# Kernel optimization log

Measured on AMD Instinct MI355X. Metric: run time of the kernel, lower is better.

Reference implementation:

```python
import jax, jax.numpy as jnp
import numpy as np

VOCAB = 100000
EMB = 100
HID = 100
CTX_LEN = 60          # must equal MAX_DESC_LEN for linear_1 to fit
FACT_LEN = 20
DESC_LEN = 60


def setup_inputs() -> dict:
    key = jax.random.key(0)
    ks = jax.random.split(key, 12)
    s = 0.05
    context = jax.random.randint(ks[0], (CTX_LEN, FACT_LEN), 1, VOCAB)
    fact_lengths = jax.random.randint(ks[1], (CTX_LEN,), 1, FACT_LEN)
    description = jax.random.randint(ks[2], (DESC_LEN,), 1, VOCAB)
    emb_ctx = jax.random.normal(ks[3], (VOCAB, EMB), jnp.float32) * s
    emb_ctx = emb_ctx.at[0].set(0.0)  # padding_idx=0
    emb_dec = jax.random.normal(ks[4], (VOCAB, EMB), jnp.float32) * s
    emb_dec = emb_dec.at[0].set(0.0)
    w1 = jax.random.normal(ks[5], (HID, CTX_LEN * HID), jnp.float32) * s
    b1 = jax.random.normal(ks[6], (HID,), jnp.float32) * s
    w_ih = jax.random.normal(ks[7], (3 * HID, EMB), jnp.float32) * s
    w_hh = jax.random.normal(ks[8], (3 * HID, HID), jnp.float32) * s
    b_ih = jax.random.normal(ks[9], (3 * HID,), jnp.float32) * s
    b_hh = jax.random.normal(ks[10], (3 * HID,), jnp.float32) * s
    w_out = jax.random.normal(ks[11], (VOCAB, HID), jnp.float32) * s
    b_out = jnp.zeros((VOCAB,), jnp.float32)
    return {"context": context, "fact_lengths": fact_lengths, "description": description,
            "emb_ctx": emb_ctx, "emb_dec": emb_dec, "w1": w1, "b1": b1,
            "w_ih": w_ih, "w_hh": w_hh, "b_ih": b_ih, "b_hh": b_hh,
            "w_out": w_out, "b_out": b_out}


def _forward(context, description, emb_ctx, emb_dec, w1, b1,
             w_ih, w_hh, b_ih, b_hh, w_out, b_out):
    # ---- InputModule: embed + positional fact encoder ----
    emb = emb_ctx[context]                       # [CTX_LEN, FACT_LEN, EMB]
    slen, elen = FACT_LEN, EMB
    s = jnp.arange(slen, dtype=jnp.float32) / (slen - 1)   # [slen]
    e = jnp.arange(elen, dtype=jnp.float32) / (elen - 1)   # [elen]
    l = 1.0 - s[:, None] - e[None, :] * (1.0 - 2.0 * s[:, None])  # [slen, elen]
    facts = jnp.sum(emb * l[None], axis=1)       # [CTX_LEN, EMB]

    # ---- initial decoder hidden from flattened facts ----
    h0 = facts.reshape(1, -1) @ w1.T + b1        # [1, HID]

    x0 = emb_dec[1][None, :]                     # SOS token embedding [1, EMB]

    def step(carry, tok):
        h, x = carry
        gi = x @ w_ih.T + b_ih                   # [1, 3H]
        gh = h @ w_hh.T + b_hh
        i_r, i_z, i_n = jnp.split(gi, 3, axis=-1)
        h_r, h_z, h_n = jnp.split(gh, 3, axis=-1)
        r = jax.nn.sigmoid(i_r + h_r)
        z = jax.nn.sigmoid(i_z + h_z)
        n = jnp.tanh(i_n + r * h_n)
        h_new = (1.0 - z) * n + z * h            # [1, HID]
        logits = h_new @ w_out.T + b_out         # [1, VOCAB]
        logp = jax.nn.log_softmax(logits, axis=-1)
        loss_t = -logp[0, tok]                   # NLLLoss, batch 1
        x_next = emb_dec[tok][None, :]           # teacher forcing
        return (h_new, x_next), loss_t

    (_, _), losses = jax.lax.scan(step, (h0, x0), description)
    return jnp.sum(losses).reshape(1)            # matches torch FloatTensor([.])


def reference(context, fact_lengths, description, emb_ctx, emb_dec, w1, b1,
              w_ih, w_hh, b_ih, b_hh, w_out, b_out):
    # fact_lengths is unused by the original forward (PositionalFactEncoder ignores it)
    return _forward(context, description, emb_ctx, emb_dec, w1, b1,
                    w_ih, w_hh, b_ih, b_hh, w_out, b_out)
```

## Files before the change

kernel.cpp:

```cpp
#include <hip/hip_runtime.h>
#include <hip/hip_bf16.h>
#include <math.h>

#define VOCAB 100000
#define EMB 100
#define HID 100
#define CTX_LEN 60
#define FACT_LEN 20
#define DESC_LEN 60
#define NCHUNK (VOCAB / 16)
#define NWAVES 1024

#define WS_FACTS 0
#define WS_X     6000
#define WS_H0    12000
#define WS_GI    12160
#define WS_H     30160
#define WS_MS    36864

typedef __attribute__((ext_vector_type(8))) short short8;
typedef __attribute__((ext_vector_type(4))) float f32x4;

static __device__ __forceinline__ unsigned short f2bf(float f) {
    union { float f; unsigned u; } x; x.f = f;
    unsigned r = (x.u + 0x7FFFu + ((x.u >> 16) & 1u)) >> 16;
    return (unsigned short)r;
}

__global__ __launch_bounds__(128) void k1_prep(const int* __restrict__ context,
                                               const int* __restrict__ desc,
                                               const float* __restrict__ emb_ctx,
                                               const float* __restrict__ emb_dec,
                                               float* __restrict__ ws,
                                               float* __restrict__ out) {
    int b = blockIdx.x, tid = threadIdx.x;
    if (b < 60) {
        __shared__ int toks[20];
        if (tid < 20) toks[tid] = context[b * 20 + tid];
        __syncthreads();
        if (tid < 100) {
            float ef = tid * (1.f / 99.f);
            float acc = 0.f;
            #pragma unroll
            for (int s = 0; s < 20; s++) {
                float sf = s * (1.f / 19.f);
                float l = 1.f - sf - ef * (1.f - 2.f * sf);
                acc = fmaf(emb_ctx[toks[s] * 100 + tid], l, acc);
            }
            ws[WS_FACTS + b * 100 + tid] = acc;
        }
    } else {
        int t = b - 60;
        int tok = (t == 0) ? 1 : desc[t - 1];
        if (tid < 100) ws[WS_X + t * 100 + tid] = emb_dec[tok * 100 + tid];
        if (b == 60 && tid == 0) out[0] = 0.f;
    }
}

__global__ __launch_bounds__(320) void k2_h0_gi(const float* __restrict__ w1,
                                                const float* __restrict__ b1,
                                                const float* __restrict__ w_ih,
                                                const float* __restrict__ b_ih,
                                                float* __restrict__ ws) {
    int b = blockIdx.x, tid = threadIdx.x;
    if (b < 100) {
        __shared__ float red[320];
        const float* facts = ws + WS_FACTS;
        const float* wr = w1 + b * 6000;
        float p = 0.f;
        for (int k = tid; k < 6000; k += 320) p = fmaf(facts[k], wr[k], p);
        red[tid] = p; __syncthreads();
        if (tid < 64) red[tid] += red[256 + tid];
        __syncthreads();
        for (int st = 128; st > 0; st >>= 1) {
            if (tid < st) red[tid] += red[tid + st];
            __syncthreads();
        }
        if (tid == 0) ws[WS_H0 + b] = red[0] + b1[b];
    } else {
        int t = b - 100;
        __shared__ float xs[100];
        if (tid < 100) xs[tid] = ws[WS_X + t * 100 + tid];
        __syncthreads();
        if (tid < 300) {
            float p = b_ih[tid];
            const float* wr = w_ih + tid * 100;
            #pragma unroll 4
            for (int k = 0; k < 100; k++) p = fmaf(wr[k], xs[k], p);
            ws[WS_GI + t * 300 + tid] = p;
        }
    }
}

__global__ __launch_bounds__(256, 1) void k3_gru(const float* __restrict__ w_hh,
                                                 const float* __restrict__ b_hh,
                                                 float* __restrict__ ws) {
    __shared__ __align__(16) float gi_lds[18000];
    __shared__ __align__(16) float H_lds[6000];
    __shared__ __align__(16) unsigned short h_bf[2][128];

    const int tid = threadIdx.x;
    const int wave = tid >> 6, lane = tid & 63;
    const int q = lane >> 4, n = lane & 15;
    const int L = lane & 31;
    const int j = wave * 32 + L;
    const bool gate_lane = (lane < 32) && (j < 100);

    short8 bfr[3][2][4];
    #pragma unroll
    for (int s = 0; s < 3; s++) {
        #pragma unroll
        for (int c = 0; c < 2; c++) {
            const int jrow = wave * 32 + c * 16 + n;
            const float* wr = w_hh + (s * 100 + jrow) * 100;
            #pragma unroll
            for (int kt = 0; kt < 4; kt++) {
                int k0 = kt * 32 + q * 8;
                float va[8];
                #pragma unroll
                for (int jj = 0; jj < 8; jj++) va[jj] = 0.f;
                if (jrow < 100) {
                    if (k0 + 4 <= 100) {
                        float4 a = *(const float4*)(wr + k0);
                        va[0] = a.x; va[1] = a.y; va[2] = a.z; va[3] = a.w;
                    }
                    if (k0 + 8 <= 100) {
                        float4 b = *(const float4*)(wr + k0 + 4);
                        va[4] = b.x; va[5] = b.y; va[6] = b.z; va[7] = b.w;
                    }
                }
                short8 f;
                #pragma unroll
                for (int jj = 0; jj < 8; jj++) f[jj] = (short)f2bf(va[jj]);
                bfr[s][c][kt] = f;
            }
        }
    }

    {
        const float4* src = (const float4*)(ws + WS_GI);
        float4* dst = (float4*)gi_lds;
        for (int k = tid; k < 4500; k += 256) dst[k] = src[k];
    }

    float hreg = 0.f, bh0 = 0.f, bh1 = 0.f, bh2 = 0.f;
    if (gate_lane) {
        hreg = ws[WS_H0 + j];
        bh0 = b_hh[j]; bh1 = b_hh[100 + j]; bh2 = b_hh[200 + j];
    }
    if (tid < 128) {
        h_bf[0][tid] = (tid < 100) ? f2bf(ws[WS_H0 + tid]) : (unsigned short)0;
        h_bf[1][tid] = 0;
    }
    __syncthreads();

    const int js = (j < 100) ? j : 0;
    for (int t = 0; t < 60; t++) {
        const int rb = t & 1;
        float gir = gi_lds[t * 300 + js];
        float giz = gi_lds[t * 300 + 100 + js];
        float gin = gi_lds[t * 300 + 200 + js];

        short8 afr[4];
        #pragma unroll
        for (int kt = 0; kt < 4; kt++)
            afr[kt] = *(const short8*)&h_bf[rb][kt * 32 + q * 8];

        f32x4 acc[3][2];
        #pragma unroll
        for (int s = 0; s < 3; s++) {
            #pragma unroll
            for (int c = 0; c < 2; c++) {
                f32x4 a = {0.f, 0.f, 0.f, 0.f};
                a = __builtin_amdgcn_mfma_f32_16x16x32_bf16(afr[0], bfr[s][c][0], a, 0, 0, 0);
                a = __builtin_amdgcn_mfma_f32_16x16x32_bf16(afr[1], bfr[s][c][1], a, 0, 0, 0);
                a = __builtin_amdgcn_mfma_f32_16x16x32_bf16(afr[2], bfr[s][c][2], a, 0, 0, 0);
                a = __builtin_amdgcn_mfma_f32_16x16x32_bf16(afr[3], bfr[s][c][3], a, 0, 0, 0);
                acc[s][c] = a;
            }
        }

        if (gate_lane) {
            const int cc = L >> 4;
            float ghr = (cc ? acc[0][1][0] : acc[0][0][0]) + bh0;
            float ghz = (cc ? acc[1][1][0] : acc[1][0][0]) + bh1;
            float ghn = (cc ? acc[2][1][0] : acc[2][0][0]) + bh2;
            float r = 1.f / (1.f + __expf(-(gir + ghr)));
            float z = 1.f / (1.f + __expf(-(giz + ghz)));
            float a2 = fmaf(r, ghn, gin);
            float tt = __expf(-2.f * fabsf(a2));
            float nn = copysignf((1.f - tt) / (1.f + tt), a2);
            hreg = (1.f - z) * nn + z * hreg;
            h_bf[rb ^ 1][j] = f2bf(hreg);
            H_lds[t * 100 + j] = hreg;
        }
        __syncthreads();
    }

    {
        const float4* src = (const float4*)H_lds;
        float4* dst = (float4*)(ws + WS_H);
        for (int k = tid; k < 1500; k += 256) dst[k] = src[k];
    }
}

__global__ __launch_bounds__(256, 1) void k4_logits(const float* __restrict__ w_out,
                                                    const float* __restrict__ b_out,
                                                    float* __restrict__ ws) {
    const float* H = ws + WS_H;
    float* ms = ws + WS_MS;
    const int lane = threadIdx.x & 63;
    const int gw = blockIdx.x * 4 + (threadIdx.x >> 6);
    const int q = lane >> 4, n = lane & 15;
    const int k_base = q * 8;

    short8 afr[4][4];
    #pragma unroll
    for (int mt = 0; mt < 4; mt++) {
        int m = mt * 16 + n;
        #pragma unroll
        for (int kt = 0; kt < 4; kt++) {
            int k0 = kt * 32 + k_base;
            float va[8];
            #pragma unroll
            for (int jj = 0; jj < 8; jj++) va[jj] = 0.f;
            if (m < 60) {
                if (k0 + 4 <= 100) {
                    float4 a = *(const float4*)(H + m * 100 + k0);
                    va[0] = a.x; va[1] = a.y; va[2] = a.z; va[3] = a.w;
                }
                if (k0 + 8 <= 100) {
                    float4 b = *(const float4*)(H + m * 100 + k0 + 4);
                    va[4] = b.x; va[5] = b.y; va[6] = b.z; va[7] = b.w;
                }
            }
            short8 f;
            #pragma unroll
            for (int jj = 0; jj < 8; jj++) f[jj] = (short)f2bf(va[jj]);
            afr[mt][kt] = f;
        }
    }

    float mS[16], sS[16];
    #pragma unroll
    for (int i = 0; i < 16; i++) { mS[i] = -3.0e38f; sS[i] = 0.f; }

    for (int c = gw; c < NCHUNK; c += NWAVES) {
        int row = c * 16 + n;
        short8 bfr[4];
        #pragma unroll
        for (int kt = 0; kt < 4; kt++) {
            int k0 = kt * 32 + k_base;
            float va[8];
            #pragma unroll
            for (int jj = 0; jj < 8; jj++) va[jj] = 0.f;
            if (k0 + 4 <= 100) {
                float4 a = *(const float4*)(w_out + row * 100 + k0);
                va[0] = a.x; va[1] = a.y; va[2] = a.z; va[3] = a.w;
            }
            if (k0 + 8 <= 100) {
                float4 b = *(const float4*)(w_out + row * 100 + k0 + 4);
                va[4] = b.x; va[5] = b.y; va[6] = b.z; va[7] = b.w;
            }
            short8 f;
            #pragma unroll
            for (int jj = 0; jj < 8; jj++) f[jj] = (short)f2bf(va[jj]);
            bfr[kt] = f;
        }
        float bo = b_out[row];
        #pragma unroll
        for (int mt = 0; mt < 4; mt++) {
            f32x4 acc = {0.f, 0.f, 0.f, 0.f};
            acc = __builtin_amdgcn_mfma_f32_16x16x32_bf16(afr[mt][0], bfr[0], acc, 0, 0, 0);
            acc = __builtin_amdgcn_mfma_f32_16x16x32_bf16(afr[mt][1], bfr[1], acc, 0, 0, 0);
            acc = __builtin_amdgcn_mfma_f32_16x16x32_bf16(afr[mt][2], bfr[2], acc, 0, 0, 0);
            acc = __builtin_amdgcn_mfma_f32_16x16x32_bf16(afr[mt][3], bfr[3], acc, 0, 0, 0);
            #pragma unroll
            for (int reg = 0; reg < 4; reg++) {
                float x = acc[reg] + bo;
                int i = mt * 4 + reg;
                float mo = mS[i];
                float mn = fmaxf(mo, x);
                sS[i] = sS[i] * __expf(mo - mn) + __expf(x - mn);
                mS[i] = mn;
            }
        }
    }

    #pragma unroll
    for (int i = 0; i < 16; i++) {
        float m = mS[i], s = sS[i];
        #pragma unroll
        for (int off = 1; off < 16; off <<= 1) {
            float m2 = __shfl_xor(m, off);
            float s2 = __shfl_xor(s, off);
            float mn = fmaxf(m, m2);
            s = s * __expf(m - mn) + s2 * __expf(m2 - mn);
            m = mn;
        }
        mS[i] = m; sS[i] = s;
    }
    if (n == 0) {
        #pragma unroll
        for (int mt = 0; mt < 4; mt++) {
            #pragma unroll
            for (int reg = 0; reg < 4; reg++) {
                int t = mt * 16 + q * 4 + reg;
                int i = mt * 4 + reg;
                if (t < 60) {
                    float2 val; val.x = mS[i]; val.y = sS[i];
                    ((float2*)ms)[t * NWAVES + gw] = val;
                }
            }
        }
    }
}

__global__ __launch_bounds__(256) void k5_final(const int* __restrict__ desc,
                                                const float* __restrict__ w_out,
                                                const float* __restrict__ b_out,
                                                const float* __restrict__ ws,
                                                float* __restrict__ out) {
    int t = blockIdx.x, tid = threadIdx.x;
    __shared__ float sm[256], ss[256], sd[256];
    const float2* ms = (const float2*)(ws + WS_MS);
    float m = -3.0e38f, s = 0.f;
    for (int i = tid; i < NWAVES; i += 256) {
        float2 p = ms[t * NWAVES + i];
        float mn = fmaxf(m, p.x);
        s = s * __expf(m - mn) + p.y * __expf(p.x - mn);
        m = mn;
    }
    sm[tid] = m; ss[tid] = s; __syncthreads();
    for (int st = 128; st > 0; st >>= 1) {
        if (tid < st) {
            float mo = sm[tid], so = ss[tid];
            float m2 = sm[tid + st], s2 = ss[tid + st];
            float mn = fmaxf(mo, m2);
            sm[tid] = mn;
            ss[tid] = so * __expf(mo - mn) + s2 * __expf(m2 - mn);
        }
        __syncthreads();
    }
    int tok = desc[t];
    float p = 0.f;
    if (tid < 100) p = ws[WS_H + t * 100 + tid] * w_out[tok * 100 + tid];
    sd[tid] = p; __syncthreads();
    for (int st = 128; st > 0; st >>= 1) {
        if (tid < st) sd[tid] += sd[tid + st];
        __syncthreads();
    }
    if (tid == 0) {
        float logit = sd[0] + b_out[tok];
        float loss = sm[0] + logf(ss[0]) - logit;
        atomicAdd(out, loss);
    }
}

extern "C" void kernel_launch(void* const* d_in, const int* in_sizes, int n_in,
                              void* d_out, int out_size, void* d_ws, size_t ws_size,
                              hipStream_t stream) {
    const int*   context = (const int*)d_in[0];
    const int*   desc    = (const int*)d_in[2];
    const float* emb_ctx = (const float*)d_in[3];
    const float* emb_dec = (const float*)d_in[4];
    const float* w1      = (const float*)d_in[5];
    const float* b1      = (const float*)d_in[6];
    const float* w_ih    = (const float*)d_in[7];
    const float* w_hh    = (const float*)d_in[8];
    const float* b_ih    = (const float*)d_in[9];
    const float* b_hh    = (const float*)d_in[10];
    const float* w_out   = (const float*)d_in[11];
    const float* b_out   = (const float*)d_in[12];
    float* out = (float*)d_out;
    float* ws  = (float*)d_ws;

    k1_prep  <<<120, 128, 0, stream>>>(context, desc, emb_ctx, emb_dec, ws, out);
    k2_h0_gi <<<160, 320, 0, stream>>>(w1, b1, w_ih, b_ih, ws);
    k3_gru   <<<1,   256, 0, stream>>>(w_hh, b_hh, ws);
    k4_logits<<<256, 256, 0, stream>>>(w_out, b_out, ws);
    k5_final <<<60,  256, 0, stream>>>(desc, w_out, b_out, ws, out);
}
```

Before: 200.3 us.

## Fuse all stages into one persistent kernel and overlap GRU with w_out conversion

Replaces the five kernel launches with a single persistent kernel of 224 blocks that separates stages with a software grid barrier built on atomics. While block 0 runs the serial GRU recurrence, the other blocks convert w_out to bf16 in MFMA fragment order in workspace, so the logits stage reads pre-packed bf16 weights instead of converting fp32 on the fly. This aims to remove launch gaps and hide the w_out conversion behind the serial GRU, at the cost of an extra write and read of a bf16 copy of w_out, a hipMemset for the barrier counter, and reliance on all blocks being co-resident.

```diff
diff --git a/kernel.cpp b/kernel.cpp
--- a/kernel.cpp
+++ b/kernel.cpp
@@ -9,14 +9,19 @@
 #define FACT_LEN 20
 #define DESC_LEN 60
 #define NCHUNK (VOCAB / 16)
-#define NWAVES 1024
-
-#define WS_FACTS 0
-#define WS_X     6000
-#define WS_H0    12000
-#define WS_GI    12160
-#define WS_H     30160
+#define GRID 224
+#define BLOCK 320
+#define WPB 5
+#define NWAVES (GRID * WPB)
+
+#define WS_BAR   0
+#define WS_FACTS 64
+#define WS_X     6144
+#define WS_H0    12288
+#define WS_GI    12416
+#define WS_H     30464
 #define WS_MS    36864
+#define WS_WBF   262144
 
 typedef __attribute__((ext_vector_type(8))) short short8;
 typedef __attribute__((ext_vector_type(4))) float f32x4;
@@ -27,15 +32,42 @@
     return (unsigned short)r;
 }
 
-__global__ __launch_bounds__(128) void k1_prep(const int* __restrict__ context,
-                                               const int* __restrict__ desc,
-                                               const float* __restrict__ emb_ctx,
-                                               const float* __restrict__ emb_dec,
-                                               float* __restrict__ ws,
-                                               float* __restrict__ out) {
-    int b = blockIdx.x, tid = threadIdx.x;
+static __device__ __forceinline__ void grid_sync(float* ws) {
+    __syncthreads();
+    if (threadIdx.x == 0) {
+        unsigned* cnt = (unsigned*)ws;
+        unsigned* gen = (unsigned*)ws + 16;
+        __threadfence();
+        unsigned g = __hip_atomic_load(gen, __ATOMIC_RELAXED, __HIP_MEMORY_SCOPE_AGENT);
+        unsigned a = __hip_atomic_fetch_add(cnt, 1u, __ATOMIC_ACQ_REL, __HIP_MEMORY_SCOPE_AGENT);
+        if (a == GRID - 1) {
+            __hip_atomic_store(cnt, 0u, __ATOMIC_RELAXED, __HIP_MEMORY_SCOPE_AGENT);
+            __hip_atomic_store(gen, g + 1u, __ATOMIC_RELEASE, __HIP_MEMORY_SCOPE_AGENT);
+        } else {
+            while (__hip_atomic_load(gen, __ATOMIC_ACQUIRE, __HIP_MEMORY_SCOPE_AGENT) == g)
+                __builtin_amdgcn_s_sleep(2);
+        }
+        __threadfence();
+    }
+    __syncthreads();
+}
+
+__global__ __launch_bounds__(BLOCK, 1) void mega(
+    const int* __restrict__ context, const int* __restrict__ desc,
+    const float* __restrict__ emb_ctx, const float* __restrict__ emb_dec,
+    const float* __restrict__ w1, const float* __restrict__ b1,
+    const float* __restrict__ w_ih, const float* __restrict__ b_ih,
+    const float* __restrict__ w_hh, const float* __restrict__ b_hh,
+    const float* __restrict__ w_out, const float* __restrict__ b_out,
+    float* __restrict__ ws, float* __restrict__ out)
+{
+    __shared__ __align__(16) float smem[24128];
+    const int b = blockIdx.x, tid = threadIdx.x;
+    const int lane = tid & 63, wave = tid >> 6;
+    const int q = lane >> 4, n = lane & 15;
+
     if (b < 60) {
-        __shared__ int toks[20];
+        int* toks = (int*)smem;
         if (tid < 20) toks[tid] = context[b * 20 + tid];
         __syncthreads();
         if (tid < 100) {
@@ -49,22 +81,17 @@
             }
             ws[WS_FACTS + b * 100 + tid] = acc;
         }
-    } else {
+    } else if (b < 120) {
         int t = b - 60;
         int tok = (t == 0) ? 1 : desc[t - 1];
         if (tid < 100) ws[WS_X + t * 100 + tid] = emb_dec[tok * 100 + tid];
-        if (b == 60 && tid == 0) out[0] = 0.f;
-    }
-}
-
-__global__ __launch_bounds__(320) void k2_h0_gi(const float* __restrict__ w1,
-                                                const float* __restrict__ b1,
-                                                const float* __restrict__ w_ih,
-                                                const float* __restrict__ b_ih,
-                                                float* __restrict__ ws) {
-    int b = blockIdx.x, tid = threadIdx.x;
+    } else if (b == 120 && tid == 0) {
+        out[0] = 0.f;
+    }
+    grid_sync(ws);
+
     if (b < 100) {
-        __shared__ float red[320];
+        float* red = smem;
         const float* facts = ws + WS_FACTS;
         const float* wr = w1 + b * 6000;
         float p = 0.f;
@@ -77,9 +104,9 @@
             __syncthreads();
         }
         if (tid == 0) ws[WS_H0 + b] = red[0] + b1[b];
-    } else {
+    } else if (b < 160) {
         int t = b - 100;
-        __shared__ float xs[100];
+        float* xs = smem;
         if (tid < 100) xs[tid] = ws[WS_X + t * 100 + tid];
         __syncthreads();
         if (tid < 300) {
@@ -90,270 +117,276 @@
             ws[WS_GI + t * 300 + tid] = p;
         }
     }
-}
-
-__global__ __launch_bounds__(256, 1) void k3_gru(const float* __restrict__ w_hh,
-                                                 const float* __restrict__ b_hh,
-                                                 float* __restrict__ ws) {
-    __shared__ __align__(16) float gi_lds[18000];
-    __shared__ __align__(16) float H_lds[6000];
-    __shared__ __align__(16) unsigned short h_bf[2][128];
-
-    const int tid = threadIdx.x;
-    const int wave = tid >> 6, lane = tid & 63;
-    const int q = lane >> 4, n = lane & 15;
-    const int L = lane & 31;
-    const int j = wave * 32 + L;
-    const bool gate_lane = (lane < 32) && (j < 100);
-
-    short8 bfr[3][2][4];
-    #pragma unroll
-    for (int s = 0; s < 3; s++) {
+    grid_sync(ws);
+
+    if (b == 0) {
+        float* gi_lds = smem;
+        float* H_lds  = smem + 18000;
+        unsigned short (*h_bf)[128] = (unsigned short (*)[128])(smem + 24000);
+        const int L = lane & 31;
+        const int j = wave * 32 + L;
+        const bool gruwave = (wave < 4);
+        const bool gate_lane = gruwave && (lane < 32) && (j < 100);
+
+        short8 bfr[3][2][4];
+        if (gruwave) {
+            #pragma unroll
+            for (int s = 0; s < 3; s++) {
+                #pragma unroll
+                for (int c = 0; c < 2; c++) {
+                    const int jrow = wave * 32 + c * 16 + n;
+                    const float* wr = w_hh + (s * 100 + jrow) * 100;
+                    #pragma unroll
+                    for (int kt = 0; kt < 4; kt++) {
+                        int k0 = kt * 32 + q * 8;
+                        float va[8];
+                        #pragma unroll
+                        for (int jj = 0; jj < 8; jj++) va[jj] = 0.f;
+                        if (jrow < 100) {
+                            if (k0 + 4 <= 100) {
+                                float4 a = *(const float4*)(wr + k0);
+                                va[0] = a.x; va[1] = a.y; va[2] = a.z; va[3] = a.w;
+                            }
+                            if (k0 + 8 <= 100) {
+                                float4 a = *(const float4*)(wr + k0 + 4);
+                                va[4] = a.x; va[5] = a.y; va[6] = a.z; va[7] = a.w;
+                            }
+                        }
+                        short8 f;
+                        #pragma unroll
+                        for (int jj = 0; jj < 8; jj++) f[jj] = (short)f2bf(va[jj]);
+                        bfr[s][c][kt] = f;
+                    }
+                }
+            }
+        }
+
+        {
+            const float4* src = (const float4*)(ws + WS_GI);
+            float4* dst = (float4*)gi_lds;
+            for (int k = tid; k < 4500; k += 320) dst[k] = src[k];
+        }
+
+        float hreg = 0.f, bh0 = 0.f, bh1 = 0.f, bh2 = 0.f;
+        if (gate_lane) {
+            hreg = ws[WS_H0 + j];
+            bh0 = b_hh[j]; bh1 = b_hh[100 + j]; bh2 = b_hh[200 + j];
+        }
+        if (tid < 128) {
+            h_bf[0][tid] = (tid < 100) ? f2bf(ws[WS_H0 + tid]) : (unsigned short)0;
+            h_bf[1][tid] = 0;
+        }
+        __syncthreads();
+
+        const int js = (gruwave && j < 100) ? j : 0;
+        for (int t = 0; t < 60; t++) {
+            const int rb = t & 1;
+            if (gruwave) {
+                float gir = gi_lds[t * 300 + js];
+                float giz = gi_lds[t * 300 + 100 + js];
+                float gin = gi_lds[t * 300 + 200 + js];
+
+                short8 afr[4];
+                #pragma unroll
+                for (int kt = 0; kt < 4; kt++)
+                    afr[kt] = *(const short8*)&h_bf[rb][kt * 32 + q * 8];
+
+                f32x4 acc[3][2];
+                #pragma unroll
+                for (int s = 0; s < 3; s++) {
+                    #pragma unroll
+                    for (int c = 0; c < 2; c++) {
+                        f32x4 a = {0.f, 0.f, 0.f, 0.f};
+                        a = __builtin_amdgcn_mfma_f32_16x16x32_bf16(afr[0], bfr[s][c][0], a, 0, 0, 0);
+                        a = __builtin_amdgcn_mfma_f32_16x16x32_bf16(afr[1], bfr[s][c][1], a, 0, 0, 0);
+                        a = __builtin_amdgcn_mfma_f32_16x16x32_bf16(afr[2], bfr[s][c][2], a, 0, 0, 0);
+                        a = __builtin_amdgcn_mfma_f32_16x16x32_bf16(afr[3], bfr[s][c][3], a, 0, 0, 0);
+                        acc[s][c] = a;
+                    }
+                }
+
+                if (gate_lane) {
+                    const int cc = L >> 4;
+                    float ghr = (cc ? acc[0][1][0] : acc[0][0][0]) + bh0;
+                    float ghz = (cc ? acc[1][1][0] : acc[1][0][0]) + bh1;
+                    float ghn = (cc ? acc[2][1][0] : acc[2][0][0]) + bh2;
+                    float r = 1.f / (1.f + __expf(-(gir + ghr)));
+                    float z = 1.f / (1.f + __expf(-(giz + ghz)));
+                    float a2 = fmaf(r, ghn, gin);
+                    float tt = __expf(-2.f * fabsf(a2));
+                    float nn = copysignf((1.f - tt) / (1.f + tt), a2);
+                    hreg = (1.f - z) * nn + z * hreg;
+                    h_bf[rb ^ 1][j] = f2bf(hreg);
+                    H_lds[t * 100 + j] = hreg;
+                }
+            }
+            __syncthreads();
+        }
+
+        {
+            const float4* src = (const float4*)H_lds;
+            float4* dst = (float4*)(ws + WS_H);
+            for (int k = tid; k < 1500; k += 320) dst[k] = src[k];
+        }
+    } else {
+        short8* wbf = (short8*)(ws + WS_WBF);
+        for (int it = (b - 1) * WPB + wave; it < NCHUNK * 4; it += (GRID - 1) * WPB) {
+            int c = it >> 2, kt = it & 3;
+            const float* wr = w_out + (c * 16 + n) * 100;
+            int k0 = kt * 32 + q * 8;
+            float va[8];
+            #pragma unroll
+            for (int jj = 0; jj < 8; jj++) va[jj] = 0.f;
+            if (k0 + 4 <= 100) {
+                float4 a = *(const float4*)(wr + k0);
+                va[0] = a.x; va[1] = a.y; va[2] = a.z; va[3] = a.w;
+            }
+            if (k0 + 8 <= 100) {
+                float4 a = *(const float4*)(wr + k0 + 4);
+                va[4] = a.x; va[5] = a.y; va[6] = a.z; va[7] = a.w;
+            }
+            short8 f;
+            #pragma unroll
+            for (int jj = 0; jj < 8; jj++) f[jj] = (short)f2bf(va[jj]);
+            wbf[(c * 4 + kt) * 64 + lane] = f;
+        }
+    }
+    grid_sync(ws);
+
+    {
+        const float* H = ws + WS_H;
+        float* ms = ws + WS_MS;
+        const short8* wbf = (const short8*)(ws + WS_WBF);
+        const int gw = b * WPB + wave;
+        const int k_base = q * 8;
+
+        short8 afr[4][4];
         #pragma unroll
-        for (int c = 0; c < 2; c++) {
-            const int jrow = wave * 32 + c * 16 + n;
-            const float* wr = w_hh + (s * 100 + jrow) * 100;
+        for (int mt = 0; mt < 4; mt++) {
+            int m = mt * 16 + n;
             #pragma unroll
             for (int kt = 0; kt < 4; kt++) {
-                int k0 = kt * 32 + q * 8;
+                int k0 = kt * 32 + k_base;
                 float va[8];
                 #pragma unroll
                 for (int jj = 0; jj < 8; jj++) va[jj] = 0.f;
-                if (jrow < 100) {
+                if (m < 60) {
                     if (k0 + 4 <= 100) {
-                        float4 a = *(const float4*)(wr + k0);
+                        float4 a = *(const float4*)(H + m * 100 + k0);
                         va[0] = a.x; va[1] = a.y; va[2] = a.z; va[3] = a.w;
                     }
                     if (k0 + 8 <= 100) {
-                        float4 b = *(const float4*)(wr + k0 + 4);
-                        va[4] = b.x; va[5] = b.y; va[6] = b.z; va[7] = b.w;
+                        float4 a = *(const float4*)(H + m * 100 + k0 + 4);
+                        va[4] = a.x; va[5] = a.y; va[6] = a.z; va[7] = a.w;
                     }
                 }
                 short8 f;
                 #pragma unroll
                 for (int jj = 0; jj < 8; jj++) f[jj] = (short)f2bf(va[jj]);
-                bfr[s][c][kt] = f;
-            }
-        }
-    }
-
-    {
-        const float4* src = (const float4*)(ws + WS_GI);
-        float4* dst = (float4*)gi_lds;
-        for (int k = tid; k < 4500; k += 256) dst[k] = src[k];
-    }
-
-    float hreg = 0.f, bh0 = 0.f, bh1 = 0.f, bh2 = 0.f;
-    if (gate_lane) {
-        hreg = ws[WS_H0 + j];
-        bh0 = b_hh[j]; bh1 = b_hh[100 + j]; bh2 = b_hh[200 + j];
-    }
-    if (tid < 128) {
-        h_bf[0][tid] = (tid < 100) ? f2bf(ws[WS_H0 + tid]) : (unsigned short)0;
-        h_bf[1][tid] = 0;
-    }
-    __syncthreads();
-
-    const int js = (j < 100) ? j : 0;
-    for (int t = 0; t < 60; t++) {
-        const int rb = t & 1;
-        float gir = gi_lds[t * 300 + js];
-        float giz = gi_lds[t * 300 + 100 + js];
-        float gin = gi_lds[t * 300 + 200 + js];
-
-        short8 afr[4];
+                afr[mt][kt] = f;
+            }
+        }
+
+        float mS[16], sS[16];
         #pragma unroll
-        for (int kt = 0; kt < 4; kt++)
-            afr[kt] = *(const short8*)&h_bf[rb][kt * 32 + q * 8];
-
-        f32x4 acc[3][2];
+        for (int i = 0; i < 16; i++) { mS[i] = -3.0e38f; sS[i] = 0.f; }
+
+        for (int c = gw; c < NCHUNK; c += NWAVES) {
+            int row = c * 16 + n;
+            short8 bw0 = wbf[(c * 4 + 0) * 64 + lane];
+            short8 bw1 = wbf[(c * 4 + 1) * 64 + lane];
+            short8 bw2 = wbf[(c * 4 + 2) * 64 + lane];
+            short8 bw3 = wbf[(c * 4 + 3) * 64 + lane];
+            float bo = b_out[row];
+            #pragma unroll
+            for (int mt = 0; mt < 4; mt++) {
+                f32x4 acc = {0.f, 0.f, 0.f, 0.f};
+                acc = __builtin_amdgcn_mfma_f32_16x16x32_bf16(afr[mt][0], bw0, acc, 0, 0, 0);
+                acc = __builtin_amdgcn_mfma_f32_16x16x32_bf16(afr[mt][1], bw1, acc, 0, 0, 0);
+                acc = __builtin_amdgcn_mfma_f32_16x16x32_bf16(afr[mt][2], bw2, acc, 0, 0, 0);
+                acc = __builtin_amdgcn_mfma_f32_16x16x32_bf16(afr[mt][3], bw3, acc, 0, 0, 0);
+                #pragma unroll
+                for (int reg = 0; reg < 4; reg++) {
+                    float x = acc[reg] + bo;
+                    int i = mt * 4 + reg;
+                    float mo = mS[i];
+                    float mn = fmaxf(mo, x);
+                    sS[i] = sS[i] * __expf(mo - mn) + __expf(x - mn);
+                    mS[i] = mn;
+                }
+            }
+        }
+
         #pragma unroll
-        for (int s = 0; s < 3; s++) {
-            #pragma unroll
-            for (int c = 0; c < 2; c++) {
-                f32x4 a = {0.f, 0.f, 0.f, 0.f};
-                a = __builtin_amdgcn_mfma_f32_16x16x32_bf16(afr[0], bfr[s][c][0], a, 0, 0, 0);
-                a = __builtin_amdgcn_mfma_f32_16x16x32_bf16(afr[1], bfr[s][c][1], a, 0, 0, 0);
-                a = __builtin_amdgcn_mfma_f32_16x16x32_bf16(afr[2], bfr[s][c][2], a, 0, 0, 0);
-                a = __builtin_amdgcn_mfma_f32_16x16x32_bf16(afr[3], bfr[s][c][3], a, 0, 0, 0);
-                acc[s][c] = a;
-            }
-        }
-
-        if (gate_lane) {
-            const int cc = L >> 4;
-            float ghr = (cc ? acc[0][1][0] : acc[0][0][0]) + bh0;
-            float ghz = (cc ? acc[1][1][0] : acc[1][0][0]) + bh1;
-            float ghn = (cc ? acc[2][1][0] : acc[2][0][0]) + bh2;
-            float r = 1.f / (1.f + __expf(-(gir + ghr)));
-            float z = 1.f / (1.f + __expf(-(giz + ghz)));
-            float a2 = fmaf(r, ghn, gin);
-            float tt = __expf(-2.f * fabsf(a2));
-            float nn = copysignf((1.f - tt) / (1.f + tt), a2);
-            hreg = (1.f - z) * nn + z * hreg;
-            h_bf[rb ^ 1][j] = f2bf(hreg);
-            H_lds[t * 100 + j] = hreg;
-        }
-        __syncthreads();
-    }
-
-    {
-        const float4* src = (const float4*)H_lds;
-        float4* dst = (float4*)(ws + WS_H);
-        for (int k = tid; k < 1500; k += 256) dst[k] = src[k];
-    }
-}
-
-__global__ __launch_bounds__(256, 1) void k4_logits(const float* __restrict__ w_out,
-                                                    const float* __restrict__ b_out,
-                                                    float* __restrict__ ws) {
-    const float* H = ws + WS_H;
-    float* ms = ws + WS_MS;
-    const int lane = threadIdx.x & 63;
-    const int gw = blockIdx.x * 4 + (threadIdx.x >> 6);
-    const int q = lane >> 4, n = lane & 15;
-    const int k_base = q * 8;
-
-    short8 afr[4][4];
-    #pragma unroll
-    for (int mt = 0; mt < 4; mt++) {
-        int m = mt * 16 + n;
-        #pragma unroll
-        for (int kt = 0; kt < 4; kt++) {
-            int k0 = kt * 32 + k_base;
-            float va[8];
-            #pragma unroll
-            for (int jj = 0; jj < 8; jj++) va[jj] = 0.f;
-            if (m < 60) {
-                if (k0 + 4 <= 100) {
-                    float4 a = *(const float4*)(H + m * 100 + k0);
-                    va[0] = a.x; va[1] = a.y; va[2] = a.z; va[3] = a.w;
-                }
-                if (k0 + 8 <= 100) {
-                    float4 b = *(const float4*)(H + m * 100 + k0 + 4);
-                    va[4] = b.x; va[5] = b.y; va[6] = b.z; va[7] = b.w;
-                }
-            }
-            short8 f;
-            #pragma unroll
-            for (int jj = 0; jj < 8; jj++) f[jj] = (short)f2bf(va[jj]);
-            afr[mt][kt] = f;
-        }
-    }
-
-    float mS[16], sS[16];
-    #pragma unroll
-    for (int i = 0; i < 16; i++) { mS[i] = -3.0e38f; sS[i] = 0.f; }
-
-    for (int c = gw; c < NCHUNK; c += NWAVES) {
-        int row = c * 16 + n;
-        short8 bfr[4];
-        #pragma unroll
-        for (int kt = 0; kt < 4; kt++) {
-            int k0 = kt * 32 + k_base;
-            float va[8];
-            #pragma unroll
-            for (int jj = 0; jj < 8; jj++) va[jj] = 0.f;
-            if (k0 + 4 <= 100) {
-                float4 a = *(const float4*)(w_out + row * 100 + k0);
-                va[0] = a.x; va[1] = a.y; va[2] = a.z; va[3] = a.w;
-            }
-            if (k0 + 8 <= 100) {
-                float4 b = *(const float4*)(w_out + row * 100 + k0 + 4);
-                va[4] = b.x; va[5] = b.y; va[6] = b.z; va[7] = b.w;
-            }
-            short8 f;
-            #pragma unroll
-            for (int jj = 0; jj < 8; jj++) f[jj] = (short)f2bf(va[jj]);
-            bfr[kt] = f;
-        }
-        float bo = b_out[row];
-        #pragma unroll
-        for (int mt = 0; mt < 4; mt++) {
-            f32x4 acc = {0.f, 0.f, 0.f, 0.f};
-            acc = __builtin_amdgcn_mfma_f32_16x16x32_bf16(afr[mt][0], bfr[0], acc, 0, 0, 0);
-            acc = __builtin_amdgcn_mfma_f32_16x16x32_bf16(afr[mt][1], bfr[1], acc, 0, 0, 0);
-            acc = __builtin_amdgcn_mfma_f32_16x16x32_bf16(afr[mt][2], bfr[2], acc, 0, 0, 0);
-            acc = __builtin_amdgcn_mfma_f32_16x16x32_bf16(afr[mt][3], bfr[3], acc, 0, 0, 0);
-            #pragma unroll
-            for (int reg = 0; reg < 4; reg++) {
-                float x = acc[reg] + bo;
-                int i = mt * 4 + reg;
-                float mo = mS[i];
-                float mn = fmaxf(mo, x);
-                sS[i] = sS[i] * __expf(mo - mn) + __expf(x - mn);
-                mS[i] = mn;
-            }
-        }
-    }
-
-    #pragma unroll
-    for (int i = 0; i < 16; i++) {
-        float m = mS[i], s = sS[i];
-        #pragma unroll
-        for (int off = 1; off < 16; off <<= 1) {
-            float m2 = __shfl_xor(m, off);
-            float s2 = __shfl_xor(s, off);
-            float mn = fmaxf(m, m2);
-            s = s * __expf(m - mn) + s2 * __expf(m2 - mn);
-            m = mn;
-        }
-        mS[i] = m; sS[i] = s;
-    }
-    if (n == 0) {
-        #pragma unroll
-        for (int mt = 0; mt < 4; mt++) {
-            #pragma unroll
-            for (int reg = 0; reg < 4; reg++) {
-                int t = mt * 16 + q * 4 + reg;
-                int i = mt * 4 + reg;
-                if (t < 60) {
-                    float2 val; val.x = mS[i]; val.y = sS[i];
-                    ((float2*)ms)[t * NWAVES + gw] = val;
-                }
-            }
-        }
-    }
-}
-
-__global__ __launch_bounds__(256) void k5_final(const int* __restrict__ desc,
-                                                const float* __restrict__ w_out,
-                                                const float* __restrict__ b_out,
-                                                const float* __restrict__ ws,
-                                                float* __restrict__ out) {
-    int t = blockIdx.x, tid = threadIdx.x;
-    __shared__ float sm[256], ss[256], sd[256];
-    const float2* ms = (const float2*)(ws + WS_MS);
-    float m = -3.0e38f, s = 0.f;
-    for (int i = tid; i < NWAVES; i += 256) {
-        float2 p = ms[t * NWAVES + i];
-        float mn = fmaxf(m, p.x);
-        s = s * __expf(m - mn) + p.y * __expf(p.x - mn);
-        m = mn;
-    }
-    sm[tid] = m; ss[tid] = s; __syncthreads();
-    for (int st = 128; st > 0; st >>= 1) {
-        if (tid < st) {
-            float mo = sm[tid], so = ss[tid];
-            float m2 = sm[tid + st], s2 = ss[tid + st];
-            float mn = fmaxf(mo, m2);
-            sm[tid] = mn;
-            ss[tid] = so * __expf(mo - mn) + s2 * __expf(m2 - mn);
-        }
-        __syncthreads();
-    }
-    int tok = desc[t];
-    float p = 0.f;
-    if (tid < 100) p = ws[WS_H + t * 100 + tid] * w_out[tok * 100 + tid];
-    sd[tid] = p; __syncthreads();
-    for (int st = 128; st > 0; st >>= 1) {
-        if (tid < st) sd[tid] += sd[tid + st];
-        __syncthreads();
-    }
-    if (tid == 0) {
-        float logit = sd[0] + b_out[tok];
-        float loss = sm[0] + logf(ss[0]) - logit;
-        atomicAdd(out, loss);
+        for (int i = 0; i < 16; i++) {
+            float m = mS[i], s = sS[i];
+            #pragma unroll
+            for (int off = 1; off < 16; off <<= 1) {
+                float m2 = __shfl_xor(m, off);
+                float s2 = __shfl_xor(s, off);
+                float mn = fmaxf(m, m2);
+                s = s * __expf(m - mn) + s2 * __expf(m2 - mn);
+                m = mn;
+            }
+            mS[i] = m; sS[i] = s;
+        }
+        if (n == 0) {
+            #pragma unroll
+            for (int mt = 0; mt < 4; mt++) {
+                #pragma unroll
+                for (int reg = 0; reg < 4; reg++) {
+                    int t = mt * 16 + q * 4 + reg;
+                    int i = mt * 4 + reg;
+                    if (t < 60) {
+                        float2 val; val.x = mS[i]; val.y = sS[i];
+                        ((float2*)ms)[t * NWAVES + gw] = val;
+                    }
+                }
+            }
+        }
+    }
+    grid_sync(ws);
+
+    if (b < 60) {
+        const int t = b;
+        float* sm  = smem;
+        float* ssm = smem + 320;
+        float* sd  = smem + 640;
+        const float2* msp = (const float2*)(ws + WS_MS);
+        float m = -3.0e38f, s = 0.f;
+        if (tid < 256) {
+            for (int i = tid; i < NWAVES; i += 256) {
+                float2 p2 = msp[t * NWAVES + i];
+                float mn = fmaxf(m, p2.x);
+                s = s * __expf(m - mn) + p2.y * __expf(p2.x - mn);
+                m = mn;
+            }
+            sm[tid] = m; ssm[tid] = s;
+        }
+        __syncthreads();
+        for (int st = 128; st > 0; st >>= 1) {
+            if (tid < st) {
+                float mo = sm[tid], so = ssm[tid];
+                float m2 = sm[tid + st], s2 = ssm[tid + st];
+                float mn = fmaxf(mo, m2);
+                sm[tid] = mn;
+                ssm[tid] = so * __expf(mo - mn) + s2 * __expf(m2 - mn);
+            }
+            __syncthreads();
+        }
+        int tok = desc[t];
+        float p = 0.f;
+        if (tid < 100) p = ws[WS_H + t * 100 + tid] * w_out[tok * 100 + tid];
+        if (tid < 256) sd[tid] = p;
+        __syncthreads();
+        for (int st = 128; st > 0; st >>= 1) {
+            if (tid < st) sd[tid] += sd[tid + st];
+            __syncthreads();
+        }
+        if (tid == 0) {
+            float logit = sd[0] + b_out[tok];
+            atomicAdd(out, sm[0] + logf(ssm[0]) - logit);
+        }
     }
 }
 
@@ -375,9 +408,7 @@
     float* out = (float*)d_out;
     float* ws  = (float*)d_ws;
 
-    k1_prep  <<<120, 128, 0, stream>>>(context, desc, emb_ctx, emb_dec, ws, out);
-    k2_h0_gi <<<160, 320, 0, stream>>>(w1, b1, w_ih, b_ih, ws);
-    k3_gru   <<<1,   256, 0, stream>>>(w_hh, b_hh, ws);
-    k4_logits<<<256, 256, 0, stream>>>(w_out, b_out, ws);
-    k5_final <<<60,  256, 0, stream>>>(desc, w_out, b_out, ws, out);
+    hipMemsetAsync(ws, 0, 128, stream);
+    mega<<<GRID, BLOCK, 0, stream>>>(context, desc, emb_ctx, emb_dec, w1, b1,
+                                     w_ih, b_ih, w_hh, b_hh, w_out, b_out, ws, out);
 }
```

Result: slower. 338.5 us (+69.0%).

## Overlap w_out bf16 conversion with serial GRU and merge prep kernels

Applied to the files above, without the earlier changes.

Merges the embedding/fact prep kernel into the h0/gi kernel, so every h0 block recomputes facts redundantly but one launch is saved. Extra blocks of the GRU kernel convert w_out into a pre-swizzled bf16 MFMA layout in the workspace while block 0 runs the serial recurrence, so the logits kernel loads ready fragments instead of converting fp32. The logits grid changes to 224 blocks, and the atomic loss sum becomes a per-step buffer plus a tiny final kernel. This adds a 20MB bf16 write and re-read, and the facts computation is repeated per h0 block.

```diff
diff --git a/kernel.cpp b/kernel.cpp
--- a/kernel.cpp
+++ b/kernel.cpp
@@ -9,14 +9,15 @@
 #define FACT_LEN 20
 #define DESC_LEN 60
 #define NCHUNK (VOCAB / 16)
-#define NWAVES 1024
-
-#define WS_FACTS 0
-#define WS_X     6000
-#define WS_H0    12000
-#define WS_GI    12160
-#define WS_H     30160
-#define WS_MS    36864
+#define GRID_BC 224
+#define NWAVES_C (GRID_BC * 4)
+
+#define WS_H0    0
+#define WS_GI    128
+#define WS_H     18176
+#define WS_LOSS  24176
+#define WS_MS    24256
+#define WS_WBF   262144
 
 typedef __attribute__((ext_vector_type(8))) short short8;
 typedef __attribute__((ext_vector_type(4))) float f32x4;
@@ -27,45 +28,35 @@
     return (unsigned short)r;
 }
 
-__global__ __launch_bounds__(128) void k1_prep(const int* __restrict__ context,
-                                               const int* __restrict__ desc,
-                                               const float* __restrict__ emb_ctx,
-                                               const float* __restrict__ emb_dec,
-                                               float* __restrict__ ws,
-                                               float* __restrict__ out) {
-    int b = blockIdx.x, tid = threadIdx.x;
-    if (b < 60) {
-        __shared__ int toks[20];
-        if (tid < 20) toks[tid] = context[b * 20 + tid];
-        __syncthreads();
-        if (tid < 100) {
-            float ef = tid * (1.f / 99.f);
+__global__ __launch_bounds__(320) void kA(const int* __restrict__ context,
+                                          const int* __restrict__ desc,
+                                          const float* __restrict__ emb_ctx,
+                                          const float* __restrict__ emb_dec,
+                                          const float* __restrict__ w1,
+                                          const float* __restrict__ b1,
+                                          const float* __restrict__ w_ih,
+                                          const float* __restrict__ b_ih,
+                                          float* __restrict__ ws) {
+    const int b = blockIdx.x, tid = threadIdx.x;
+    if (b < 100) {
+        __shared__ int toks[1200];
+        __shared__ float facts[6000];
+        __shared__ float red[320];
+        for (int i = tid; i < 1200; i += 320) toks[i] = context[i];
+        __syncthreads();
+        for (int idx = tid; idx < 6000; idx += 320) {
+            int fb = idx / 100, e = idx - fb * 100;
+            float ef = e * (1.f / 99.f);
             float acc = 0.f;
             #pragma unroll
             for (int s = 0; s < 20; s++) {
                 float sf = s * (1.f / 19.f);
                 float l = 1.f - sf - ef * (1.f - 2.f * sf);
-                acc = fmaf(emb_ctx[toks[s] * 100 + tid], l, acc);
-            }
-            ws[WS_FACTS + b * 100 + tid] = acc;
-        }
-    } else {
-        int t = b - 60;
-        int tok = (t == 0) ? 1 : desc[t - 1];
-        if (tid < 100) ws[WS_X + t * 100 + tid] = emb_dec[tok * 100 + tid];
-        if (b == 60 && tid == 0) out[0] = 0.f;
-    }
-}
-
-__global__ __launch_bounds__(320) void k2_h0_gi(const float* __restrict__ w1,
-                                                const float* __restrict__ b1,
-                                                const float* __restrict__ w_ih,
-                                                const float* __restrict__ b_ih,
-                                                float* __restrict__ ws) {
-    int b = blockIdx.x, tid = threadIdx.x;
-    if (b < 100) {
-        __shared__ float red[320];
-        const float* facts = ws + WS_FACTS;
+                acc = fmaf(emb_ctx[toks[fb * 20 + s] * 100 + e], l, acc);
+            }
+            facts[idx] = acc;
+        }
+        __syncthreads();
         const float* wr = w1 + b * 6000;
         float p = 0.f;
         for (int k = tid; k < 6000; k += 320) p = fmaf(facts[k], wr[k], p);
@@ -78,9 +69,10 @@
         }
         if (tid == 0) ws[WS_H0 + b] = red[0] + b1[b];
     } else {
-        int t = b - 100;
+        const int t = b - 100;
+        const int tok = (t == 0) ? 1 : desc[t - 1];
         __shared__ float xs[100];
-        if (tid < 100) xs[tid] = ws[WS_X + t * 100 + tid];
+        if (tid < 100) xs[tid] = emb_dec[tok * 100 + tid];
         __syncthreads();
         if (tid < 300) {
             float p = b_ih[tid];
@@ -92,16 +84,43 @@
     }
 }
 
-__global__ __launch_bounds__(256, 1) void k3_gru(const float* __restrict__ w_hh,
-                                                 const float* __restrict__ b_hh,
-                                                 float* __restrict__ ws) {
-    __shared__ __align__(16) float gi_lds[18000];
-    __shared__ __align__(16) float H_lds[6000];
-    __shared__ __align__(16) unsigned short h_bf[2][128];
-
-    const int tid = threadIdx.x;
-    const int wave = tid >> 6, lane = tid & 63;
+__global__ __launch_bounds__(256, 1) void kB(const float* __restrict__ w_hh,
+                                             const float* __restrict__ b_hh,
+                                             const float* __restrict__ w_out,
+                                             float* __restrict__ ws) {
+    __shared__ __align__(16) float smem[24128];
+    const int b = blockIdx.x, tid = threadIdx.x;
+    const int lane = tid & 63, wave = tid >> 6;
     const int q = lane >> 4, n = lane & 15;
+
+    if (b != 0) {
+        short8* wbf = (short8*)(ws + WS_WBF);
+        for (int it = (b - 1) * 4 + wave; it < NCHUNK * 4; it += 223 * 4) {
+            int c = it >> 2, kt = it & 3;
+            const float* wr = w_out + (c * 16 + n) * 100;
+            int k0 = kt * 32 + q * 8;
+            float va[8];
+            #pragma unroll
+            for (int jj = 0; jj < 8; jj++) va[jj] = 0.f;
+            if (k0 + 4 <= 100) {
+                float4 a = *(const float4*)(wr + k0);
+                va[0] = a.x; va[1] = a.y; va[2] = a.z; va[3] = a.w;
+            }
+            if (k0 + 8 <= 100) {
+                float4 a = *(const float4*)(wr + k0 + 4);
+                va[4] = a.x; va[5] = a.y; va[6] = a.z; va[7] = a.w;
+            }
+            short8 f;
+            #pragma unroll
+            for (int jj = 0; jj < 8; jj++) f[jj] = (short)f2bf(va[jj]);
+            wbf[(c * 4 + kt) * 64 + lane] = f;
+        }
+        return;
+    }
+
+    float* gi_lds = smem;
+    float* H_lds  = smem + 18000;
+    unsigned short (*h_bf)[128] = (unsigned short (*)[128])(smem + 24000);
     const int L = lane & 31;
     const int j = wave * 32 + L;
     const bool gate_lane = (lane < 32) && (j < 100);
@@ -125,8 +144,8 @@
                         va[0] = a.x; va[1] = a.y; va[2] = a.z; va[3] = a.w;
                     }
                     if (k0 + 8 <= 100) {
-                        float4 b = *(const float4*)(wr + k0 + 4);
-                        va[4] = b.x; va[5] = b.y; va[6] = b.z; va[7] = b.w;
+                        float4 a = *(const float4*)(wr + k0 + 4);
+                        va[4] = a.x; va[5] = a.y; va[6] = a.z; va[7] = a.w;
                     }
                 }
                 short8 f;
@@ -204,14 +223,15 @@
     }
 }
 
-__global__ __launch_bounds__(256, 1) void k4_logits(const float* __restrict__ w_out,
-                                                    const float* __restrict__ b_out,
-                                                    float* __restrict__ ws) {
+__global__ __launch_bounds__(256, 1) void kC(const float* __restrict__ b_out,
+                                             float* __restrict__ ws) {
     const float* H = ws + WS_H;
     float* ms = ws + WS_MS;
-    const int lane = threadIdx.x & 63;
-    const int gw = blockIdx.x * 4 + (threadIdx.x >> 6);
+    const short8* wbf = (const short8*)(ws + WS_WBF);
+    const int tid = threadIdx.x;
+    const int lane = tid & 63, wave = tid >> 6;
     const int q = lane >> 4, n = lane & 15;
+    const int gw = blockIdx.x * 4 + wave;
     const int k_base = q * 8;
 
     short8 afr[4][4];
@@ -230,8 +250,8 @@
                     va[0] = a.x; va[1] = a.y; va[2] = a.z; va[3] = a.w;
                 }
                 if (k0 + 8 <= 100) {
-                    float4 b = *(const float4*)(H + m * 100 + k0 + 4);
-                    va[4] = b.x; va[5] = b.y; va[6] = b.z; va[7] = b.w;
+                    float4 a = *(const float4*)(H + m * 100 + k0 + 4);
+                    va[4] = a.x; va[5] = a.y; va[6] = a.z; va[7] = a.w;
                 }
             }
             short8 f;
@@ -245,36 +265,20 @@
     #pragma unroll
     for (int i = 0; i < 16; i++) { mS[i] = -3.0e38f; sS[i] = 0.f; }
 
-    for (int c = gw; c < NCHUNK; c += NWAVES) {
+    for (int c = gw; c < NCHUNK; c += NWAVES_C) {
         int row = c * 16 + n;
-        short8 bfr[4];
-        #pragma unroll
-        for (int kt = 0; kt < 4; kt++) {
-            int k0 = kt * 32 + k_base;
-            float va[8];
-            #pragma unroll
-            for (int jj = 0; jj < 8; jj++) va[jj] = 0.f;
-            if (k0 + 4 <= 100) {
-                float4 a = *(const float4*)(w_out + row * 100 + k0);
-                va[0] = a.x; va[1] = a.y; va[2] = a.z; va[3] = a.w;
-            }
-            if (k0 + 8 <= 100) {
-                float4 b = *(const float4*)(w_out + row * 100 + k0 + 4);
-                va[4] = b.x; va[5] = b.y; va[6] = b.z; va[7] = b.w;
-            }
-            short8 f;
-            #pragma unroll
-            for (int jj = 0; jj < 8; jj++) f[jj] = (short)f2bf(va[jj]);
-            bfr[kt] = f;
-        }
+        short8 bw0 = wbf[(c * 4 + 0) * 64 + lane];
+        short8 bw1 = wbf[(c * 4 + 1) * 64 + lane];
+        short8 bw2 = wbf[(c * 4 + 2) * 64 + lane];
+        short8 bw3 = wbf[(c * 4 + 3) * 64 + lane];
         float bo = b_out[row];
         #pragma unroll
         for (int mt = 0; mt < 4; mt++) {
             f32x4 acc = {0.f, 0.f, 0.f, 0.f};
-            acc = __builtin_amdgcn_mfma_f32_16x16x32_bf16(afr[mt][0], bfr[0], acc, 0, 0, 0);
-            acc = __builtin_amdgcn_mfma_f32_16x16x32_bf16(afr[mt][1], bfr[1], acc, 0, 0, 0);
-            acc = __builtin_amdgcn_mfma_f32_16x16x32_bf16(afr[mt][2], bfr[2], acc, 0, 0, 0);
-            acc = __builtin_amdgcn_mfma_f32_16x16x32_bf16(afr[mt][3], bfr[3], acc, 0, 0, 0);
+            acc = __builtin_amdgcn_mfma_f32_16x16x32_bf16(afr[mt][0], bw0, acc, 0, 0, 0);
+            acc = __builtin_amdgcn_mfma_f32_16x16x32_bf16(afr[mt][1], bw1, acc, 0, 0, 0);
+            acc = __builtin_amdgcn_mfma_f32_16x16x32_bf16(afr[mt][2], bw2, acc, 0, 0, 0);
+            acc = __builtin_amdgcn_mfma_f32_16x16x32_bf16(afr[mt][3], bw3, acc, 0, 0, 0);
             #pragma unroll
             for (int reg = 0; reg < 4; reg++) {
                 float x = acc[reg] + bo;
@@ -309,26 +313,25 @@
                 int i = mt * 4 + reg;
                 if (t < 60) {
                     float2 val; val.x = mS[i]; val.y = sS[i];
-                    ((float2*)ms)[t * NWAVES + gw] = val;
+                    ((float2*)ms)[t * NWAVES_C + gw] = val;
                 }
             }
         }
     }
 }
 
-__global__ __launch_bounds__(256) void k5_final(const int* __restrict__ desc,
-                                                const float* __restrict__ w_out,
-                                                const float* __restrict__ b_out,
-                                                const float* __restrict__ ws,
-                                                float* __restrict__ out) {
-    int t = blockIdx.x, tid = threadIdx.x;
+__global__ __launch_bounds__(256) void kD(const int* __restrict__ desc,
+                                          const float* __restrict__ w_out,
+                                          const float* __restrict__ b_out,
+                                          float* __restrict__ ws) {
+    const int t = blockIdx.x, tid = threadIdx.x;
     __shared__ float sm[256], ss[256], sd[256];
-    const float2* ms = (const float2*)(ws + WS_MS);
+    const float2* msp = (const float2*)(ws + WS_MS);
     float m = -3.0e38f, s = 0.f;
-    for (int i = tid; i < NWAVES; i += 256) {
-        float2 p = ms[t * NWAVES + i];
-        float mn = fmaxf(m, p.x);
-        s = s * __expf(m - mn) + p.y * __expf(p.x - mn);
+    for (int i = tid; i < NWAVES_C; i += 256) {
+        float2 p2 = msp[t * NWAVES_C + i];
+        float mn = fmaxf(m, p2.x);
+        s = s * __expf(m - mn) + p2.y * __expf(p2.x - mn);
         m = mn;
     }
     sm[tid] = m; ss[tid] = s; __syncthreads();
@@ -342,7 +345,7 @@
         }
         __syncthreads();
     }
-    int tok = desc[t];
+    const int tok = desc[t];
     float p = 0.f;
     if (tid < 100) p = ws[WS_H + t * 100 + tid] * w_out[tok * 100 + tid];
     sd[tid] = p; __syncthreads();
@@ -352,8 +355,16 @@
     }
     if (tid == 0) {
         float logit = sd[0] + b_out[tok];
-        float loss = sm[0] + logf(ss[0]) - logit;
-        atomicAdd(out, loss);
+        ws[WS_LOSS + t] = sm[0] + logf(ss[0]) - logit;
+    }
+}
+
+__global__ __launch_bounds__(64) void kE(const float* __restrict__ ws,
+                                         float* __restrict__ out) {
+    if (threadIdx.x == 0) {
+        float tot = 0.f;
+        for (int t = 0; t < 60; t++) tot += ws[WS_LOSS + t];
+        out[0] = tot;
     }
 }
 
@@ -375,9 +386,9 @@
     float* out = (float*)d_out;
     float* ws  = (float*)d_ws;
 
-    k1_prep  <<<120, 128, 0, stream>>>(context, desc, emb_ctx, emb_dec, ws, out);
-    k2_h0_gi <<<160, 320, 0, stream>>>(w1, b1, w_ih, b_ih, ws);
-    k3_gru   <<<1,   256, 0, stream>>>(w_hh, b_hh, ws);
-    k4_logits<<<256, 256, 0, stream>>>(w_out, b_out, ws);
-    k5_final <<<60,  256, 0, stream>>>(desc, w_out, b_out, ws, out);
-}
+    kA<<<160, 320, 0, stream>>>(context, desc, emb_ctx, emb_dec, w1, b1, w_ih, b_ih, ws);
+    kB<<<GRID_BC, 256, 0, stream>>>(w_hh, b_hh, w_out, ws);
+    kC<<<GRID_BC, 256, 0, stream>>>(b_out, ws);
+    kD<<<60, 256, 0, stream>>>(desc, w_out, b_out, ws);
+    kE<<<1, 64, 0, stream>>>(ws, out);
+}
```

Measured after the change: 207.1 us. +3.4%, slower.
